# Performance work log

Measured on AMD Instinct MI355X. Metric: run time of the kernel, lower is better.

Reference implementation:

```python
import jax, jax.numpy as jnp
import numpy as np

NUM_CLASSES = 16384
FEAT_DIM = 1024
ALPHA = 0.5


def setup_inputs() -> dict:
    key = jax.random.key(0)
    k1, k2, k3 = jax.random.split(key, 3)
    y_true = jax.random.randint(k1, (NUM_CLASSES,), 0, NUM_CLASSES, dtype=jnp.int32)
    y_pred = jax.random.normal(k2, (NUM_CLASSES, FEAT_DIM), dtype=jnp.float32)
    centers = jax.random.normal(k3, (NUM_CLASSES, FEAT_DIM), dtype=jnp.float32)
    return {"y_true": y_true, "y_pred": y_pred, "centers": centers}


def reference(y_true, y_pred, centers):
    # gather current centers per sample: [B, D]
    delta_centers = centers[y_true] - y_pred
    # per-class counts, gathered back per sample (tf.math.bincount semantics,
    # static length = NUM_CLASSES since all indices < NUM_CLASSES)
    counts = jnp.bincount(y_true, length=NUM_CLASSES)
    per_sample_counts = counts[y_true].astype(y_pred.dtype)  # [B]
    delta_centers = ALPHA * delta_centers / (per_sample_counts[:, None] + 1.0)
    # original code does an elementwise assign_sub (requires B == num_classes)
    new_centers = centers - delta_centers
    # MSE between features and the freshly-updated gathered centers
    diff = y_pred - new_centers[y_true]
    loss = jnp.mean(jnp.square(diff))
    return loss
```

## Files before the change

kernel.cpp:

```cpp
#include <hip/hip_runtime.h>

#define B 16384
#define D 1024
#define CL_ALPHA 0.5f
#define ROWS 4
#define NBLK (B / ROWS)

__global__ void count_kernel(const int* __restrict__ y_true, int* __restrict__ counts) {
    int i = blockIdx.x * blockDim.x + threadIdx.x;
    if (i < B) atomicAdd(&counts[y_true[i]], 1);
}

__global__ void prep_kernel(const int* __restrict__ y_true,
                            const int* __restrict__ counts,
                            int* __restrict__ k_arr,
                            float* __restrict__ inv_arr) {
    int i = blockIdx.x * blockDim.x + threadIdx.x;
    if (i >= B) return;
    int j = y_true[i];
    int k = y_true[j];
    k_arr[i] = k;
    inv_arr[i] = CL_ALPHA / ((float)counts[k] + 1.0f);
}

__global__ __launch_bounds__(256) void loss_kernel(const int* __restrict__ y_true,
                                                   const float* __restrict__ y_pred,
                                                   const float* __restrict__ centers,
                                                   const int* __restrict__ k_arr,
                                                   const float* __restrict__ inv_arr,
                                                   float* __restrict__ partials) {
    const int base = blockIdx.x * ROWS;
    const int t = threadIdx.x;

    int   js[ROWS], ks[ROWS];
    float invs[ROWS];
    #pragma unroll
    for (int r = 0; r < ROWS; ++r) {
        js[r]   = y_true[base + r];
        ks[r]   = k_arr[base + r];
        invs[r] = inv_arr[base + r];
    }

    float4 a[ROWS], bj[ROWS], ck[ROWS], yj[ROWS];
    #pragma unroll
    for (int r = 0; r < ROWS; ++r) {
        a[r]  = ((const float4*)(y_pred  + (size_t)(base + r) * D))[t];
        bj[r] = ((const float4*)(centers + (size_t)js[r]   * D))[t];
        ck[r] = ((const float4*)(centers + (size_t)ks[r]   * D))[t];
        yj[r] = ((const float4*)(y_pred  + (size_t)js[r]   * D))[t];
    }

    float acc = 0.0f;
    #pragma unroll
    for (int r = 0; r < ROWS; ++r) {
        const float inv = invs[r];
        float dx = a[r].x - bj[r].x + inv * (ck[r].x - yj[r].x);
        float dy = a[r].y - bj[r].y + inv * (ck[r].y - yj[r].y);
        float dz = a[r].z - bj[r].z + inv * (ck[r].z - yj[r].z);
        float dw = a[r].w - bj[r].w + inv * (ck[r].w - yj[r].w);
        acc += dx * dx + dy * dy + dz * dz + dw * dw;
    }

    #pragma unroll
    for (int off = 32; off > 0; off >>= 1)
        acc += __shfl_down(acc, off, 64);

    __shared__ float smem[4];
    const int lane = t & 63;
    const int wave = t >> 6;
    if (lane == 0) smem[wave] = acc;
    __syncthreads();
    if (t == 0)
        partials[blockIdx.x] = smem[0] + smem[1] + smem[2] + smem[3];
}

__global__ __launch_bounds__(1024) void finalize_kernel(const float* __restrict__ partials,
                                                        float* __restrict__ out) {
    const int t = threadIdx.x;
    const float4* p4 = (const float4*)partials;
    float4 v = p4[t];
    float acc = v.x + v.y + v.z + v.w;

    #pragma unroll
    for (int off = 32; off > 0; off >>= 1)
        acc += __shfl_down(acc, off, 64);

    __shared__ float smem[16];
    const int lane = t & 63;
    const int wave = t >> 6;
    if (lane == 0) smem[wave] = acc;
    __syncthreads();
    if (t == 0) {
        float s = 0.0f;
        #pragma unroll
        for (int w = 0; w < 16; ++w) s += smem[w];
        out[0] = s * (1.0f / ((float)B * (float)D));
    }
}

extern "C" void kernel_launch(void* const* d_in, const int* in_sizes, int n_in,
                              void* d_out, int out_size, void* d_ws, size_t ws_size,
                              hipStream_t stream) {
    const int*   y_true  = (const int*)d_in[0];
    const float* y_pred  = (const float*)d_in[1];
    const float* centers = (const float*)d_in[2];
    float* out = (float*)d_out;

    int*   counts   = (int*)d_ws;
    int*   k_arr    = counts + B;
    float* inv_arr  = (float*)(k_arr + B);
    float* partials = inv_arr + B;

    hipMemsetAsync(counts, 0, B * sizeof(int), stream);

    count_kernel<<<256, 64, 0, stream>>>(y_true, counts);
    prep_kernel<<<256, 64, 0, stream>>>(y_true, counts, k_arr, inv_arr);
    loss_kernel<<<NBLK, 256, 0, stream>>>(y_true, y_pred, centers, k_arr, inv_arr, partials);
    finalize_kernel<<<1, 1024, 0, stream>>>(partials, out);
}
```

Measured before the change: 161.3 us.

## Stage loss-kernel row loads through LDS with direct global-to-LDS loads

The loss kernel now has each wave fetch one of the four source row types (y_pred, gathered centers, centers[k], gathered y_pred) for two rows directly into LDS using global_load_lds, then all threads compute from LDS. ROWS drops from 4 to 2, doubling the block count, and the finalize kernel reads twice as many partials. The intent is to issue larger asynchronous transfers that bypass registers and to raise the number of blocks in flight. In exchange it adds 32KB of LDS per block, an extra barrier, and LDS read traffic.

```diff
diff --git a/kernel.cpp b/kernel.cpp
--- a/kernel.cpp
+++ b/kernel.cpp
@@ -3,8 +3,12 @@
 #define B 16384
 #define D 1024
 #define CL_ALPHA 0.5f
-#define ROWS 4
+#define ROWS 2
 #define NBLK (B / ROWS)
+
+#define GLD16(gsrc, ldst) \
+  __builtin_amdgcn_global_load_lds((const __attribute__((address_space(1))) void*)(gsrc), \
+                                   (__attribute__((address_space(3))) void*)(ldst), 16, 0, 0)
 
 __global__ void count_kernel(const int* __restrict__ y_true, int* __restrict__ counts) {
     int i = blockIdx.x * blockDim.x + threadIdx.x;
@@ -29,35 +33,59 @@
                                                    const int* __restrict__ k_arr,
                                                    const float* __restrict__ inv_arr,
                                                    float* __restrict__ partials) {
+    __shared__ float lds[8 * D];
+
     const int base = blockIdx.x * ROWS;
-    const int t = threadIdx.x;
+    const int t    = threadIdx.x;
+    const int wave = t >> 6;
+    const int lane = t & 63;
 
-    int   js[ROWS], ks[ROWS];
-    float invs[ROWS];
+    const int j0 = y_true[base];
+    const int j1 = y_true[base + 1];
+    const int k0 = k_arr[base];
+    const int k1 = k_arr[base + 1];
+
+    const float *rA, *rB;
+    if (wave == 0)      { rA = y_pred  + (size_t)base * D;       rB = y_pred  + (size_t)(base + 1) * D; }
+    else if (wave == 1) { rA = centers + (size_t)j0 * D;         rB = centers + (size_t)j1 * D; }
+    else if (wave == 2) { rA = centers + (size_t)k0 * D;         rB = centers + (size_t)k1 * D; }
+    else                { rA = y_pred  + (size_t)j0 * D;         rB = y_pred  + (size_t)j1 * D; }
+
+    float* ldsA = lds + (size_t)(wave * 2) * D;
+    float* ldsB = ldsA + D;
     #pragma unroll
-    for (int r = 0; r < ROWS; ++r) {
-        js[r]   = y_true[base + r];
-        ks[r]   = k_arr[base + r];
-        invs[r] = inv_arr[base + r];
+    for (int seg = 0; seg < 4; ++seg) {
+        GLD16(rA + seg * 256 + lane * 4, ldsA + seg * 256);
+        GLD16(rB + seg * 256 + lane * 4, ldsB + seg * 256);
     }
 
-    float4 a[ROWS], bj[ROWS], ck[ROWS], yj[ROWS];
-    #pragma unroll
-    for (int r = 0; r < ROWS; ++r) {
-        a[r]  = ((const float4*)(y_pred  + (size_t)(base + r) * D))[t];
-        bj[r] = ((const float4*)(centers + (size_t)js[r]   * D))[t];
-        ck[r] = ((const float4*)(centers + (size_t)ks[r]   * D))[t];
-        yj[r] = ((const float4*)(y_pred  + (size_t)js[r]   * D))[t];
+    const float inv0 = inv_arr[base];
+    const float inv1 = inv_arr[base + 1];
+
+    __syncthreads();
+
+    const float4* L = (const float4*)lds;
+    float acc;
+    {
+        float4 a  = L[0 * 256 + t];
+        float4 bj = L[2 * 256 + t];
+        float4 ck = L[4 * 256 + t];
+        float4 yj = L[6 * 256 + t];
+        float dx = a.x - bj.x + inv0 * (ck.x - yj.x);
+        float dy = a.y - bj.y + inv0 * (ck.y - yj.y);
+        float dz = a.z - bj.z + inv0 * (ck.z - yj.z);
+        float dw = a.w - bj.w + inv0 * (ck.w - yj.w);
+        acc = dx * dx + dy * dy + dz * dz + dw * dw;
     }
-
-    float acc = 0.0f;
-    #pragma unroll
-    for (int r = 0; r < ROWS; ++r) {
-        const float inv = invs[r];
-        float dx = a[r].x - bj[r].x + inv * (ck[r].x - yj[r].x);
-        float dy = a[r].y - bj[r].y + inv * (ck[r].y - yj[r].y);
-        float dz = a[r].z - bj[r].z + inv * (ck[r].z - yj[r].z);
-        float dw = a[r].w - bj[r].w + inv * (ck[r].w - yj[r].w);
+    {
+        float4 a  = L[1 * 256 + t];
+        float4 bj = L[3 * 256 + t];
+        float4 ck = L[5 * 256 + t];
+        float4 yj = L[7 * 256 + t];
+        float dx = a.x - bj.x + inv1 * (ck.x - yj.x);
+        float dy = a.y - bj.y + inv1 * (ck.y - yj.y);
+        float dz = a.z - bj.z + inv1 * (ck.z - yj.z);
+        float dw = a.w - bj.w + inv1 * (ck.w - yj.w);
         acc += dx * dx + dy * dy + dz * dz + dw * dw;
     }
 
@@ -65,21 +93,20 @@
     for (int off = 32; off > 0; off >>= 1)
         acc += __shfl_down(acc, off, 64);
 
-    __shared__ float smem[4];
-    const int lane = t & 63;
-    const int wave = t >> 6;
-    if (lane == 0) smem[wave] = acc;
+    __syncthreads();
+    if (lane == 0) lds[wave] = acc;
     __syncthreads();
     if (t == 0)
-        partials[blockIdx.x] = smem[0] + smem[1] + smem[2] + smem[3];
+        partials[blockIdx.x] = lds[0] + lds[1] + lds[2] + lds[3];
 }
 
 __global__ __launch_bounds__(1024) void finalize_kernel(const float* __restrict__ partials,
                                                         float* __restrict__ out) {
     const int t = threadIdx.x;
     const float4* p4 = (const float4*)partials;
-    float4 v = p4[t];
-    float acc = v.x + v.y + v.z + v.w;
+    float4 v0 = p4[t];
+    float4 v1 = p4[t + 1024];
+    float acc = v0.x + v0.y + v0.z + v0.w + v1.x + v1.y + v1.z + v1.w;
 
     #pragma unroll
     for (int off = 32; off > 0; off >>= 1)
```

Result: no change. 161.1 us (-0.1%).
